# Optimization experiments

Measured on AMD Instinct MI355X. Metric: run time of the kernel, lower is better.

Reference implementation:

```python
import jax, jax.numpy as jnp
import numpy as np

B, N1, R12, R23 = 1, 4096, 4, 4
N2, N3 = N1 * R12, N1 * R12 * R23
D, F, H, NCLS, K = 1024, 512, 256, 4, 256


def setup_inputs() -> dict:
    key = jax.random.key(0)
    ks = jax.random.split(key, 10)
    s = 0.02
    return {
        "x1": jax.random.normal(ks[0], (B, N1, D), jnp.float32),
        "x2": jax.random.normal(ks[1], (B, N2, D), jnp.float32),
        "x3": jax.random.normal(ks[2], (B, N3, D), jnp.float32),
        # 3 fc layers (low/mid/high mag): Linear(D->F)
        "fcW": (jax.random.normal(ks[3], (3, D, F), jnp.float32) * s),
        "fcb": jnp.zeros((3, F), jnp.float32),
        # 5 gated-attention modules: 0=ga_low,1=ga_mid,2=ga_high,3=aux_low,4=aux_mid
        "gaWa": (jax.random.normal(ks[4], (5, F, H), jnp.float32) * s),
        "gaba": jnp.zeros((5, H), jnp.float32),
        "gaWb": (jax.random.normal(ks[5], (5, F, H), jnp.float32) * s),
        "gabb": jnp.zeros((5, H), jnp.float32),
        "gaWc": (jax.random.normal(ks[6], (5, H, 1), jnp.float32) * s),
        "gabc": jnp.zeros((5, 1), jnp.float32),
        "Wh": (jax.random.normal(ks[7], (F, NCLS), jnp.float32) * s),
        "bh": jnp.zeros((NCLS,), jnp.float32),
        "k_sample": K,
    }


def _ga(x, i, Wa, ba, Wb, bb, Wc, bc):
    # GatedAttention: tanh branch * sigmoid branch -> Linear(H->1); returns (B,N)
    a = jnp.tanh(x @ Wa[i] + ba[i])
    g = jax.nn.sigmoid(x @ Wb[i] + bb[i])
    return ((a * g) @ Wc[i] + bc[i])[..., 0]


def _block_gather(x, idx, ratio):
    # Equivalent to einsum('bkn,bnd->bkd', kron(one_hot(idx), eye(ratio)), x):
    # pick contiguous blocks of `ratio` rows for each selected coarse index.
    b, n, d = x.shape
    xb = x.reshape(b, n // ratio, ratio, d)
    out = jnp.take_along_axis(xb, idx[:, :, None, None], axis=1)  # (B,k,ratio,D)
    return out.reshape(b, idx.shape[1] * ratio, d)


def reference(x1, x2, x3, fcW, fcb, gaWa, gaba, gaWb, gabb, gaWc, gabc, Wh, bh, k_sample):
    ga = (gaWa, gaba, gaWb, gabb, gaWc, gabc)
    n1, n2, n3 = x1.shape[1], x2.shape[1], x3.shape[1]

    # --- low mag ---
    h1 = jax.nn.relu(x1 @ fcW[0] + fcb[0])                    # (B,N1,F)
    A1 = jax.nn.softmax(_ga(h1, 0, *ga), axis=-1)             # (B,N1)
    M1 = jnp.einsum('bn,bnf->bf', A1, h1)                     # (B,F)
    A1_aux = jax.nn.softmax(_ga(h1, 3, *ga), axis=-1)
    k1 = min(n1, int(k_sample))
    idx1 = jnp.sort(jax.lax.top_k(A1_aux, k1)[1], axis=-1)    # (B,k1)

    # zoom: gather selected blocks from mid and high mag features
    x2s = _block_gather(x2, idx1, n2 // n1)                   # (B,k1*R12,D)
    x3s = _block_gather(x3, idx1, n3 // n1)                   # (B,k1*R12*R23,D)

    # --- mid mag ---
    h2 = jax.nn.relu(x2s @ fcW[1] + fcb[1])
    A2 = jax.nn.softmax(_ga(h2, 1, *ga), axis=-1)
    M2 = jnp.einsum('bn,bnf->bf', A2, h2)
    A2_aux = jax.nn.softmax(_ga(h2, 4, *ga), axis=-1)
    k2 = min(h2.shape[1], int(k_sample))
    idx2 = jnp.sort(jax.lax.top_k(A2_aux, k2)[1], axis=-1)

    x3s2 = _block_gather(x3s, idx2, n3 // n2)                 # (B,k2*R23,D)

    # --- high mag ---
    h3 = jax.nn.relu(x3s2 @ fcW[2] + fcb[2])
    A3 = jax.nn.softmax(_ga(h3, 2, *ga), axis=-1)
    M3 = jnp.einsum('bn,bnf->bf', A3, h3)

    M = M1 + M2 + M3                                           # (B,F)
    logits = M @ Wh + bh                                       # (B,NCLS)
    return logits
```

## Files before the change

### kernel.cpp

```cpp
#include <hip/hip_runtime.h>
#include <hip/hip_bf16.h>
#include <math.h>


typedef __attribute__((ext_vector_type(8))) short short8;
typedef __attribute__((ext_vector_type(4))) float float4a;

__device__ __forceinline__ ushort f2bf(float f) {
    unsigned u = __float_as_uint(f);
    return (ushort)((u + 0x7fffu + ((u >> 16) & 1u)) >> 16);
}
__device__ __forceinline__ uint pk2(float a, float b) {
    __hip_bfloat162 t = __float22bfloat162_rn(make_float2(a, b));
    uint u; __builtin_memcpy(&u, &t, 4); return u;
}
__device__ __forceinline__ float aload(const float* p) {
    return __hip_atomic_load(p, __ATOMIC_RELAXED, __HIP_MEMORY_SCOPE_AGENT);
}

template<int SPLIT>
__global__ __launch_bounds__(256) void zm_hgemm(
    const float* __restrict__ A, int lda,
    const int* __restrict__ rowmap,
    const ushort* __restrict__ Bt,
    const float* __restrict__ bias,
    float* __restrict__ Cf, ushort* __restrict__ Cb, int ldc, int K)
{
    __shared__ ushort As[128 * 40];
    __shared__ ushort Bs[64 * 40];
    const int tid = threadIdx.x;
    const int brow = blockIdx.y << 7;
    const int bcol = blockIdx.x << 6;
    const int kbeg = SPLIT ? ((int)blockIdx.z << 8) : 0;
    const int kend = SPLIT ? kbeg + 256 : K;

    const int sr = tid >> 1;
    const int sk = (tid & 1) << 4;
    int arow = brow + sr;
    if (rowmap) arow = rowmap[arow];
    const float* Ap = A + (size_t)arow * lda;

    const int bn = tid >> 2;
    const int bk = (tid & 3) << 3;
    const ushort* Bp = Bt + (size_t)(bcol + bn) * K + bk;

    const int w = tid >> 6;
    const int wm = (w >> 1) << 6;
    const int wn = (w & 1) << 5;
    const int lane = tid & 63;
    const int lm = lane & 15;
    const int lq = lane >> 4;

    float4a acc[4][2] = {};

    for (int k0 = kbeg; k0 < kend; k0 += 32) {
        const float* ap = Ap + k0 + sk;
        float4 v0 = *(const float4*)(ap);
        float4 v1 = *(const float4*)(ap + 4);
        float4 v2 = *(const float4*)(ap + 8);
        float4 v3 = *(const float4*)(ap + 12);
        uint4 p0, p1;
        p0.x = pk2(v0.x, v0.y); p0.y = pk2(v0.z, v0.w);
        p0.z = pk2(v1.x, v1.y); p0.w = pk2(v1.z, v1.w);
        p1.x = pk2(v2.x, v2.y); p1.y = pk2(v2.z, v2.w);
        p1.z = pk2(v3.x, v3.y); p1.w = pk2(v3.z, v3.w);
        *(uint4*)&As[sr * 40 + sk]     = p0;
        *(uint4*)&As[sr * 40 + sk + 8] = p1;
        *(uint4*)&Bs[bn * 40 + bk] = *(const uint4*)(Bp + k0);
        __syncthreads();
        short8 afr[4], bfr[2];
#pragma unroll
        for (int mt = 0; mt < 4; mt++)
            afr[mt] = *(const short8*)&As[(wm + mt * 16 + lm) * 40 + lq * 8];
#pragma unroll
        for (int nt = 0; nt < 2; nt++)
            bfr[nt] = *(const short8*)&Bs[(wn + nt * 16 + lm) * 40 + lq * 8];
#pragma unroll
        for (int mt = 0; mt < 4; mt++)
#pragma unroll
            for (int nt = 0; nt < 2; nt++)
                acc[mt][nt] = __builtin_amdgcn_mfma_f32_16x16x32_bf16(
                    afr[mt], bfr[nt], acc[mt][nt], 0, 0, 0);
        __syncthreads();
    }

#pragma unroll
    for (int mt = 0; mt < 4; mt++) {
#pragma unroll
        for (int nt = 0; nt < 2; nt++) {
            int gc = bcol + wn + nt * 16 + lm;
            float bv = bias[gc];
            if (SPLIT && blockIdx.z != 0) bv = 0.0f;
#pragma unroll
            for (int r = 0; r < 4; r++) {
                int gr = brow + wm + mt * 16 + lq * 4 + r;
                float v = acc[mt][nt][r] + bv;
                if (SPLIT) {
                    atomicAdd(&Cf[(size_t)gr * ldc + gc], v);
                } else {
                    v = fmaxf(v, 0.0f);
                    Cf[(size_t)gr * ldc + gc] = v;
                    Cb[(size_t)gr * ldc + gc] = f2bf(v);
                }
            }
        }
    }
}

template<int AMODE>
__global__ __launch_bounds__(256) void zm_sgemm(
    const void* __restrict__ Av, int lda,
    const ushort* __restrict__ Bt,
    const float* __restrict__ bint,
    const float* __restrict__ wc0, const float* __restrict__ wc1,
    float* __restrict__ sMain, float* __restrict__ sAux,
    float* __restrict__ statsOut, int* __restrict__ cnt2, int lastBlk)
{
    __shared__ ushort As[64 * 40];
    __shared__ ushort Bs[64 * 40];
    __shared__ float part[4][64];
    const int tid = threadIdx.x;
    const int brow = blockIdx.y << 6;
    const int bcol = blockIdx.x << 6;

    const int sr = tid >> 2;
    const int sk = (tid & 3) << 3;
    const float*  Af = (const float*)Av;
    const ushort* Ab = (const ushort*)Av;
    const ushort* Bp = Bt + (size_t)(bcol + sr) * 512 + sk;

    const int w = tid >> 6;
    const int wn = w << 4;
    const int lane = tid & 63;
    const int lm = lane & 15;
    const int lq = lane >> 4;

    float4a acc[4] = {};

    for (int k0 = 0; k0 < 512; k0 += 32) {
        if (AMODE == 0) {
            *(uint4*)&As[sr * 40 + sk] =
                *(const uint4*)(Ab + (size_t)(brow + sr) * lda + k0 + sk);
        } else {
            const float* ap = Af + (size_t)(brow + sr) * lda + k0 + sk;
            float4 v0 = *(const float4*)ap;
            float4 v1 = *(const float4*)(ap + 4);
            v0.x = fmaxf(v0.x, 0.f); v0.y = fmaxf(v0.y, 0.f);
            v0.z = fmaxf(v0.z, 0.f); v0.w = fmaxf(v0.w, 0.f);
            v1.x = fmaxf(v1.x, 0.f); v1.y = fmaxf(v1.y, 0.f);
            v1.z = fmaxf(v1.z, 0.f); v1.w = fmaxf(v1.w, 0.f);
            uint4 pk;
            pk.x = pk2(v0.x, v0.y); pk.y = pk2(v0.z, v0.w);
            pk.z = pk2(v1.x, v1.y); pk.w = pk2(v1.z, v1.w);
            *(uint4*)&As[sr * 40 + sk] = pk;
        }
        *(uint4*)&Bs[sr * 40 + sk] = *(const uint4*)(Bp + k0);
        __syncthreads();
        short8 bfr = *(const short8*)&Bs[(wn + lm) * 40 + lq * 8];
#pragma unroll
        for (int mt = 0; mt < 4; mt++) {
            short8 afr = *(const short8*)&As[(mt * 16 + lm) * 40 + lq * 8];
            acc[mt] = __builtin_amdgcn_mfma_f32_16x16x32_bf16(afr, bfr, acc[mt], 0, 0, 0);
        }
        __syncthreads();
    }

    const int gc = bcol + wn + lm;
    const float* wcp = (gc >= 512) ? wc1 : wc0;
    const float wcv = wcp[(gc & 511) >> 1];
    const float bv = bint[gc];
    const bool odd = (gc & 1);
    float* sp = (bcol >= 512) ? sAux : sMain;

#pragma unroll
    for (int mt = 0; mt < 4; mt++) {
        float red[4];
#pragma unroll
        for (int r = 0; r < 4; r++) {
            float v = acc[mt][r] + bv;
            float x = odd ? (1.0f / (1.0f + expf(-v))) : tanhf(v);
            float prt = __shfl_xor(x, 1);
            float ctr = odd ? 0.0f : (x * prt * wcv);
            ctr += __shfl_xor(ctr, 1);
            ctr += __shfl_xor(ctr, 2);
            ctr += __shfl_xor(ctr, 4);
            ctr += __shfl_xor(ctr, 8);
            red[r] = ctr;
        }
        if (lm == 0) {
#pragma unroll
            for (int r = 0; r < 4; r++) part[w][mt * 16 + lq * 4 + r] = red[r];
        }
    }
    __syncthreads();
    if (tid < 64) {
        float tot = part[0][tid] + part[1][tid] + part[2][tid] + part[3][tid];
        atomicAdd(&sp[brow + tid], tot);
    }

    if (statsOut) {
        __threadfence();
        __shared__ int lastf;
        if (tid == 0)
            lastf = (__hip_atomic_fetch_add(cnt2, 1, __ATOMIC_ACQ_REL,
                                            __HIP_MEMORY_SCOPE_AGENT) == lastBlk);
        __syncthreads();
        if (lastf) {
            float* red = (float*)part;
            float vv[4];
            float mx = -3.4e38f;
#pragma unroll
            for (int j = 0; j < 4; j++) {
                vv[j] = aload(&sMain[tid + j * 256]);
                mx = fmaxf(mx, vv[j]);
            }
            red[tid] = mx; __syncthreads();
            for (int o = 128; o > 0; o >>= 1) {
                if (tid < o) red[tid] = fmaxf(red[tid], red[tid + o]);
                __syncthreads();
            }
            mx = red[0]; __syncthreads();
            float z = 0.0f;
#pragma unroll
            for (int j = 0; j < 4; j++) z += expf(vv[j] - mx);
            red[tid] = z; __syncthreads();
            for (int o = 128; o > 0; o >>= 1) {
                if (tid < o) red[tid] += red[tid + o];
                __syncthreads();
            }
            if (tid == 0) { statsOut[0] = mx; statsOut[1] = red[0]; }
        }
    }
}

__global__ __launch_bounds__(1024) void zm_topk(
    const float* __restrict__ sa, const float* __restrict__ sm, int n,
    const int* __restrict__ idx_prev,
    int* __restrict__ idx_out, int* __restrict__ rm_out,
    float* __restrict__ stOut)
{
    __shared__ float redf[1024];
    __shared__ int hist[256];
    __shared__ int idxbuf[256];
    __shared__ int wsum[16];
    __shared__ int bcastB, bcastAbove;
    const int bs = 1024;
    const int tid = threadIdx.x;

    if (blockIdx.x == 1) {
        float mx = -3.4e38f;
        for (int i = tid; i < n; i += bs) mx = fmaxf(mx, sm[i]);
        redf[tid] = mx; __syncthreads();
        for (int o = 512; o > 0; o >>= 1) {
            if (tid < o) redf[tid] = fmaxf(redf[tid], redf[tid + o]);
            __syncthreads();
        }
        mx = redf[0]; __syncthreads();
        float z = 0.0f;
        for (int i = tid; i < n; i += bs) z += expf(sm[i] - mx);
        redf[tid] = z; __syncthreads();
        for (int o = 512; o > 0; o >>= 1) {
            if (tid < o) redf[tid] += redf[tid + o];
            __syncthreads();
        }
        if (tid == 0) { stOut[0] = mx; stOut[1] = redf[0]; }
        return;
    }

    const int ept = n >> 10;
    const int lane = tid & 63;
    unsigned key[4];
#pragma unroll
    for (int e = 0; e < 4; e++) key[e] = 0;
    for (int e = 0; e < ept; e++) {
        unsigned u = __float_as_uint(sa[tid * ept + e]);
        key[e] = (u & 0x80000000u) ? ~u : (u | 0x80000000u);
    }

    unsigned prefix = 0;
    int remaining = 256;
    for (int pass = 0; pass < 4; pass++) {
        const int shift = 24 - pass * 8;
        if (tid < 256) hist[tid] = 0;
        __syncthreads();
        for (int e = 0; e < ept; e++) {
            unsigned k = key[e];
            bool ok = (pass == 0) || ((k >> (shift + 8)) == (prefix >> (shift + 8)));
            if (ok) atomicAdd(&hist[(k >> shift) & 0xff], 1);
        }
        __syncthreads();
        if (tid < 64) {
            int h0 = hist[lane * 4 + 0], h1 = hist[lane * 4 + 1];
            int h2 = hist[lane * 4 + 2], h3 = hist[lane * 4 + 3];
            int q = h0 + h1 + h2 + h3;
            int suf = q;
#pragma unroll
            for (int o = 1; o < 64; o <<= 1) {
                int v = __shfl_down(suf, o);
                if (lane + o < 64) suf += v;
            }
            int above = suf - q;
            int c3 = above + h3;
            int c2 = c3 + h2;
            int c1 = c2 + h1;
            int c0 = c1 + h0;
            int cc[4]  = {c0, c1, c2, c3};
            int nxt[4] = {c1, c2, c3, above};
#pragma unroll
            for (int j = 0; j < 4; j++)
                if (cc[j] >= remaining && nxt[j] < remaining) {
                    bcastB = lane * 4 + j;
                    bcastAbove = nxt[j];
                }
        }
        __syncthreads();
        prefix |= ((unsigned)bcastB) << shift;
        remaining -= bcastAbove;
        __syncthreads();
    }
    const unsigned T = prefix;
    const int m = remaining;

    int gt = 0, eq = 0;
    for (int e = 0; e < ept; e++) { gt += (key[e] > T); eq += (key[e] == T); }
    int packed = (gt << 16) | eq;
    int incl = packed;
#pragma unroll
    for (int o = 1; o < 64; o <<= 1) {
        int v = __shfl_up(incl, o);
        if (lane >= o) incl += v;
    }
    if (lane == 63) wsum[tid >> 6] = incl;
    __syncthreads();
    if (tid < 64) {
        int v = (tid < 16) ? wsum[tid] : 0;
        int s = v;
#pragma unroll
        for (int o = 1; o < 16; o <<= 1) {
            int t2 = __shfl_up(s, o);
            if (tid >= o) s += t2;
        }
        if (tid < 16) wsum[tid] = s - v;
    }
    __syncthreads();
    int base = wsum[tid >> 6] + incl - packed;
    int gt_before = base >> 16;
    int eq_before = base & 0xffff;
    for (int e = 0; e < ept; e++) {
        if (key[e] > T) {
            int eqa = (eq_before < m) ? eq_before : m;
            idxbuf[gt_before + eqa] = tid * ept + e;
            gt_before++;
        } else if (key[e] == T) {
            if (eq_before < m) idxbuf[gt_before + eq_before] = tid * ept + e;
            eq_before++;
        }
    }
    __syncthreads();
    if (tid < 256) idx_out[tid] = idxbuf[tid];
    int t = idxbuf[tid >> 2] * 4 + (tid & 3);
    rm_out[tid] = idx_prev ? (idx_prev[t >> 4] * 16 + (t & 15)) : t;
}

__global__ __launch_bounds__(256) void zm_prep(
    const float* __restrict__ fcW,
    const float* __restrict__ gaWa, const float* __restrict__ gaWb,
    const float* __restrict__ gaba, const float* __restrict__ gabb,
    ushort* __restrict__ fc_t, ushort* __restrict__ gint,
    float* __restrict__ bint, float4* __restrict__ zbase, int zn4)
{
    const int b = blockIdx.x;
    const int tid = threadIdx.x;
    if (b >= 2817) {
        float4 z4 = make_float4(0.f, 0.f, 0.f, 0.f);
        for (int i = (b - 2817) * 256 + tid; i < zn4; i += 64 * 256)
            zbase[i] = z4;
        return;
    }
    if (b == 2816) {
        for (int i = tid; i < 2560; i += 256) {
            int n, head;
            if (i < 1024)      { n = i;        head = (n >> 9) ? 3 : 0; }
            else if (i < 2048) { n = i - 1024; head = (n >> 9) ? 4 : 1; }
            else               { n = i - 2048; head = 2; }
            int h = (n & 511) >> 1;
            const float* src = (n & 1) ? gabb : gaba;
            bint[i] = src[head * 256 + h];
        }
        return;
    }
    __shared__ ushort tile[32][33];
    const int c = tid & 31, r8 = tid >> 5;
    if (b < 1536) {
        int mat = b >> 9, rem = b & 511;
        int tk = rem >> 4, tn = rem & 15;
        const float* src = fcW + (size_t)mat * 1024 * 512;
        ushort* dst = fc_t + (size_t)mat * 512 * 1024;
        int k0 = tk * 32, n0 = tn * 32;
#pragma unroll
        for (int it = 0; it < 4; it++) {
            int r = r8 + it * 8;
            tile[r][c] = f2bf(src[(size_t)(k0 + r) * 512 + n0 + c]);
        }
        __syncthreads();
#pragma unroll
        for (int it = 0; it < 4; it++) {
            int r = r8 + it * 8;
            dst[(size_t)(n0 + r) * 1024 + k0 + c] = tile[c][r];
        }
    } else {
        int idx = b - 1536;
        int mat = idx >> 7, rem = idx & 127;
        int tk = rem >> 3, th = rem & 7;
        int head = mat >> 1, br = mat & 1;
        const float* src = (br ? gaWb : gaWa) + (size_t)head * 512 * 256;
        ushort* dstb; int off;
        if (head == 0)      { dstb = gint;              off = 0;   }
        else if (head == 1) { dstb = gint + 1024 * 512; off = 0;   }
        else if (head == 2) { dstb = gint + 2048 * 512; off = 0;   }
        else if (head == 3) { dstb = gint;              off = 512; }
        else                { dstb = gint + 1024 * 512; off = 512; }
        int k0 = tk * 32, h0 = th * 32;
#pragma unroll
        for (int it = 0; it < 4; it++) {
            int r = r8 + it * 8;
            tile[r][c] = f2bf(src[(size_t)(k0 + r) * 256 + h0 + c]);
        }
        __syncthreads();
#pragma unroll
        for (int it = 0; it < 4; it++) {
            int r = r8 + it * 8;
            dstb[(size_t)(off + 2 * (h0 + r) + br) * 512 + k0 + c] = tile[c][r];
        }
    }
}

__global__ __launch_bounds__(256) void zm_final(
    const float* __restrict__ h1f, const float* __restrict__ h2f,
    const float* __restrict__ h3f,
    const float* __restrict__ s1, const float* __restrict__ s2,
    const float* __restrict__ s3,
    const float* __restrict__ st, float* __restrict__ Mbuf,
    int* __restrict__ cnt,
    const float* __restrict__ Wh, const float* __restrict__ bh,
    float* __restrict__ out)
{
    const int tid = threadIdx.x;
    const int b = blockIdx.x;
    const float* h; const float* s; const float* stp; int r0, rl;
    if (b < 64)      { h = h1f; s = s1; stp = st;     r0 = b * 64;        rl = 0; }
    else if (b < 80) { h = h2f; s = s2; stp = st + 2; r0 = (b - 64) * 64; rl = 1; }
    else             { h = h3f; s = s3; stp = st + 4; r0 = (b - 80) * 64; rl = 1; }
    const float mx = stp[0];
    const float invZ = 1.0f / stp[1];
    float a0 = 0.0f, a1 = 0.0f;
    for (int r = 0; r < 64; r++) {
        int n = r0 + r;
        float wgt = expf(s[n] - mx) * invZ;
        float v0 = h[(size_t)n * 512 + tid];
        float v1 = h[(size_t)n * 512 + 256 + tid];
        if (rl) { v0 = fmaxf(v0, 0.f); v1 = fmaxf(v1, 0.f); }
        a0 += wgt * v0; a1 += wgt * v1;
    }
    atomicAdd(&Mbuf[tid], a0);
    atomicAdd(&Mbuf[tid + 256], a1);
    __threadfence();
    __shared__ int lastf;
    if (tid == 0)
        lastf = (__hip_atomic_fetch_add(cnt, 1, __ATOMIC_ACQ_REL,
                                        __HIP_MEMORY_SCOPE_AGENT) == 95);
    __syncthreads();
    if (lastf) {
        const int c = tid >> 6, lane = tid & 63;
        float pacc = 0.0f;
        for (int f = lane; f < 512; f += 64)
            pacc += aload(&Mbuf[f]) * Wh[f * 4 + c];
        for (int o = 32; o > 0; o >>= 1) pacc += __shfl_down(pacc, o);
        if (lane == 0) out[c] = pacc + bh[c];
    }
}

extern "C" void kernel_launch(void* const* d_in, const int* in_sizes, int n_in,
                              void* d_out, int out_size, void* d_ws, size_t ws_size,
                              hipStream_t stream)
{
    const float* x1   = (const float*)d_in[0];
    const float* x2   = (const float*)d_in[1];
    const float* x3   = (const float*)d_in[2];
    const float* fcW  = (const float*)d_in[3];
    const float* fcb  = (const float*)d_in[4];
    const float* gaWa = (const float*)d_in[5];
    const float* gaba = (const float*)d_in[6];
    const float* gaWb = (const float*)d_in[7];
    const float* gabb = (const float*)d_in[8];
    const float* gaWc = (const float*)d_in[9];
    const float* Wh   = (const float*)d_in[11];
    const float* bh   = (const float*)d_in[12];
    float* out = (float*)d_out;

    char* p = (char*)d_ws;
    float*  h1f  = (float*)p;
    ushort* h1b  = (ushort*)(p + 8388608);
    ushort* fc_t = (ushort*)(p + 12582912);
    ushort* gint = (ushort*)(p + 15728640);
    float*  bint = (float*)(p + 18350080);
    float*  st   = (float*)(p + 18360320);
    int*    idx1 = (int*)(p + 18360352);
    int*    idx2 = (int*)(p + 18361376);
    int*    rm2  = (int*)(p + 18362400);
    int*    rm3  = (int*)(p + 18366496);
    char*   zbase = p + 18370592;
    float*  h2f  = (float*)zbase;
    float*  h3f  = (float*)(zbase + 2097152);
    float*  s1   = (float*)(zbase + 4194304);
    float*  s1a  = (float*)(zbase + 4210688);
    float*  s2   = (float*)(zbase + 4227072);
    float*  s2a  = (float*)(zbase + 4231168);
    float*  s3   = (float*)(zbase + 4235264);
    float*  Mbuf = (float*)(zbase + 4239360);
    int*    cnt  = (int*)(zbase + 4241408);
    const int ZN4 = 4241424 / 16;

    zm_prep<<<2881, 256, 0, stream>>>(fcW, gaWa, gaWb, gaba, gabb,
                                      fc_t, gint, bint, (float4*)zbase, ZN4);
    zm_hgemm<0><<<dim3(8, 32), 256, 0, stream>>>(x1, 1024, nullptr, fc_t, fcb,
                                                 h1f, h1b, 512, 1024);
    zm_sgemm<0><<<dim3(16, 64), 256, 0, stream>>>(h1b, 512, gint, bint,
                                                  gaWc, gaWc + 3 * 256,
                                                  s1, s1a, nullptr, nullptr, 0);
    zm_topk<<<2, 1024, 0, stream>>>(s1a, s1, 4096, nullptr, idx1, rm2, st);
    zm_hgemm<1><<<dim3(8, 8, 4), 256, 0, stream>>>(x2, 1024, rm2,
                                                   fc_t + 512 * 1024, fcb + 512,
                                                   h2f, nullptr, 512, 1024);
    zm_sgemm<1><<<dim3(16, 16), 256, 0, stream>>>(h2f, 512, gint + 1024 * 512,
                                                  bint + 1024,
                                                  gaWc + 256, gaWc + 4 * 256,
                                                  s2, s2a, nullptr, nullptr, 0);
    zm_topk<<<2, 1024, 0, stream>>>(s2a, s2, 1024, idx1, idx2, rm3, st + 2);
    zm_hgemm<1><<<dim3(8, 8, 4), 256, 0, stream>>>(x3, 1024, rm3,
                                                   fc_t + 2 * 512 * 1024, fcb + 1024,
                                                   h3f, nullptr, 512, 1024);
    zm_sgemm<1><<<dim3(8, 16), 256, 0, stream>>>(h3f, 512, gint + 2048 * 512,
                                                 bint + 2048,
                                                 gaWc + 2 * 256, gaWc + 2 * 256,
                                                 s3, s3, st + 4, cnt + 1, 127);
    zm_final<<<96, 256, 0, stream>>>(h1f, h2f, h3f, s1, s2, s3, st, Mbuf, cnt,
                                     Wh, bh, out);
}
```

Before: 540.4 us.

## Double-buffer GEMM tiles, fuse top-k into score GEMM, vectorize prep, widen final

Both GEMM kernels now use double-buffered shared-memory tiles and prefetch the next K slice into registers, which removes one barrier per iteration. The separate top-k/softmax-stats kernel is folded into the tail of the score GEMM: the last-arriving block does the radix select and builds the row maps, saving two launches. The weight-transpose prep switches to float4 loads and ushort4 stores, and the final reduction uses twice as many blocks with half the rows each. The fused top-k now runs on a single 256-thread block instead of 1024 threads, so that serial tail may take longer; the new completion counters (cnt+2, cnt+3) must sit inside the zeroed region.

```diff
diff --git a/kernel.cpp b/kernel.cpp
--- a/kernel.cpp
+++ b/kernel.cpp
@@ -26,13 +26,14 @@
     const float* __restrict__ bias,
     float* __restrict__ Cf, ushort* __restrict__ Cb, int ldc, int K)
 {
-    __shared__ ushort As[128 * 40];
-    __shared__ ushort Bs[64 * 40];
+    __shared__ ushort As[2][128 * 40];
+    __shared__ ushort Bs[2][64 * 40];
     const int tid = threadIdx.x;
     const int brow = blockIdx.y << 7;
     const int bcol = blockIdx.x << 6;
     const int kbeg = SPLIT ? ((int)blockIdx.z << 8) : 0;
     const int kend = SPLIT ? kbeg + 256 : K;
+    const int nsteps = (kend - kbeg) >> 5;
 
     const int sr = tid >> 1;
     const int sk = (tid & 1) << 4;
@@ -53,35 +54,48 @@
 
     float4a acc[4][2] = {};
 
-    for (int k0 = kbeg; k0 < kend; k0 += 32) {
-        const float* ap = Ap + k0 + sk;
-        float4 v0 = *(const float4*)(ap);
-        float4 v1 = *(const float4*)(ap + 4);
-        float4 v2 = *(const float4*)(ap + 8);
-        float4 v3 = *(const float4*)(ap + 12);
+    float4 v0, v1, v2, v3; uint4 bld;
+    {
+        const float* ap = Ap + kbeg + sk;
+        v0 = *(const float4*)(ap);
+        v1 = *(const float4*)(ap + 4);
+        v2 = *(const float4*)(ap + 8);
+        v3 = *(const float4*)(ap + 12);
+        bld = *(const uint4*)(Bp + kbeg);
+    }
+
+    for (int s = 0; s < nsteps; s++) {
+        const int cur = s & 1;
         uint4 p0, p1;
         p0.x = pk2(v0.x, v0.y); p0.y = pk2(v0.z, v0.w);
         p0.z = pk2(v1.x, v1.y); p0.w = pk2(v1.z, v1.w);
         p1.x = pk2(v2.x, v2.y); p1.y = pk2(v2.z, v2.w);
         p1.z = pk2(v3.x, v3.y); p1.w = pk2(v3.z, v3.w);
-        *(uint4*)&As[sr * 40 + sk]     = p0;
-        *(uint4*)&As[sr * 40 + sk + 8] = p1;
-        *(uint4*)&Bs[bn * 40 + bk] = *(const uint4*)(Bp + k0);
-        __syncthreads();
+        *(uint4*)&As[cur][sr * 40 + sk]     = p0;
+        *(uint4*)&As[cur][sr * 40 + sk + 8] = p1;
+        *(uint4*)&Bs[cur][bn * 40 + bk] = bld;
+        __syncthreads();
+        if (s + 1 < nsteps) {
+            const float* ap = Ap + kbeg + ((s + 1) << 5) + sk;
+            v0 = *(const float4*)(ap);
+            v1 = *(const float4*)(ap + 4);
+            v2 = *(const float4*)(ap + 8);
+            v3 = *(const float4*)(ap + 12);
+            bld = *(const uint4*)(Bp + kbeg + ((s + 1) << 5));
+        }
         short8 afr[4], bfr[2];
 #pragma unroll
         for (int mt = 0; mt < 4; mt++)
-            afr[mt] = *(const short8*)&As[(wm + mt * 16 + lm) * 40 + lq * 8];
+            afr[mt] = *(const short8*)&As[cur][(wm + mt * 16 + lm) * 40 + lq * 8];
 #pragma unroll
         for (int nt = 0; nt < 2; nt++)
-            bfr[nt] = *(const short8*)&Bs[(wn + nt * 16 + lm) * 40 + lq * 8];
+            bfr[nt] = *(const short8*)&Bs[cur][(wn + nt * 16 + lm) * 40 + lq * 8];
 #pragma unroll
         for (int mt = 0; mt < 4; mt++)
 #pragma unroll
             for (int nt = 0; nt < 2; nt++)
                 acc[mt][nt] = __builtin_amdgcn_mfma_f32_16x16x32_bf16(
                     afr[mt], bfr[nt], acc[mt][nt], 0, 0, 0);
-        __syncthreads();
     }
 
 #pragma unroll
@@ -107,17 +121,19 @@
     }
 }
 
-template<int AMODE>
+template<int AMODE, int NS, int DOTOPK>
 __global__ __launch_bounds__(256) void zm_sgemm(
     const void* __restrict__ Av, int lda,
     const ushort* __restrict__ Bt,
     const float* __restrict__ bint,
     const float* __restrict__ wc0, const float* __restrict__ wc1,
     float* __restrict__ sMain, float* __restrict__ sAux,
+    const int* __restrict__ idx_prev,
+    int* __restrict__ idx_out, int* __restrict__ rm_out,
     float* __restrict__ statsOut, int* __restrict__ cnt2, int lastBlk)
 {
-    __shared__ ushort As[64 * 40];
-    __shared__ ushort Bs[64 * 40];
+    __shared__ ushort As[2][64 * 40];
+    __shared__ ushort Bs[2][64 * 40];
     __shared__ float part[4][64];
     const int tid = threadIdx.x;
     const int brow = blockIdx.y << 6;
@@ -137,14 +153,22 @@
 
     float4a acc[4] = {};
 
-    for (int k0 = 0; k0 < 512; k0 += 32) {
+    uint4 aldu; float4 af0, af1; uint4 bld;
+    if (AMODE == 0) {
+        aldu = *(const uint4*)(Ab + (size_t)(brow + sr) * lda + sk);
+    } else {
+        const float* ap = Af + (size_t)(brow + sr) * lda + sk;
+        af0 = *(const float4*)ap;
+        af1 = *(const float4*)(ap + 4);
+    }
+    bld = *(const uint4*)(Bp);
+
+    for (int s = 0; s < 16; s++) {
+        const int cur = s & 1;
         if (AMODE == 0) {
-            *(uint4*)&As[sr * 40 + sk] =
-                *(const uint4*)(Ab + (size_t)(brow + sr) * lda + k0 + sk);
+            *(uint4*)&As[cur][sr * 40 + sk] = aldu;
         } else {
-            const float* ap = Af + (size_t)(brow + sr) * lda + k0 + sk;
-            float4 v0 = *(const float4*)ap;
-            float4 v1 = *(const float4*)(ap + 4);
+            float4 v0 = af0, v1 = af1;
             v0.x = fmaxf(v0.x, 0.f); v0.y = fmaxf(v0.y, 0.f);
             v0.z = fmaxf(v0.z, 0.f); v0.w = fmaxf(v0.w, 0.f);
             v1.x = fmaxf(v1.x, 0.f); v1.y = fmaxf(v1.y, 0.f);
@@ -152,17 +176,27 @@
             uint4 pk;
             pk.x = pk2(v0.x, v0.y); pk.y = pk2(v0.z, v0.w);
             pk.z = pk2(v1.x, v1.y); pk.w = pk2(v1.z, v1.w);
-            *(uint4*)&As[sr * 40 + sk] = pk;
-        }
-        *(uint4*)&Bs[sr * 40 + sk] = *(const uint4*)(Bp + k0);
-        __syncthreads();
-        short8 bfr = *(const short8*)&Bs[(wn + lm) * 40 + lq * 8];
+            *(uint4*)&As[cur][sr * 40 + sk] = pk;
+        }
+        *(uint4*)&Bs[cur][sr * 40 + sk] = bld;
+        __syncthreads();
+        if (s + 1 < 16) {
+            const int k1 = (s + 1) << 5;
+            if (AMODE == 0) {
+                aldu = *(const uint4*)(Ab + (size_t)(brow + sr) * lda + k1 + sk);
+            } else {
+                const float* ap = Af + (size_t)(brow + sr) * lda + k1 + sk;
+                af0 = *(const float4*)ap;
+                af1 = *(const float4*)(ap + 4);
+            }
+            bld = *(const uint4*)(Bp + k1);
+        }
+        short8 bfr = *(const short8*)&Bs[cur][(wn + lm) * 40 + lq * 8];
 #pragma unroll
         for (int mt = 0; mt < 4; mt++) {
-            short8 afr = *(const short8*)&As[(mt * 16 + lm) * 40 + lq * 8];
+            short8 afr = *(const short8*)&As[cur][(mt * 16 + lm) * 40 + lq * 8];
             acc[mt] = __builtin_amdgcn_mfma_f32_16x16x32_bf16(afr, bfr, acc[mt], 0, 0, 0);
         }
-        __syncthreads();
     }
 
     const int gc = bcol + wn + lm;
@@ -198,168 +232,139 @@
         atomicAdd(&sp[brow + tid], tot);
     }
 
-    if (statsOut) {
-        __threadfence();
-        __shared__ int lastf;
-        if (tid == 0)
-            lastf = (__hip_atomic_fetch_add(cnt2, 1, __ATOMIC_ACQ_REL,
-                                            __HIP_MEMORY_SCOPE_AGENT) == lastBlk);
-        __syncthreads();
-        if (lastf) {
-            float* red = (float*)part;
-            float vv[4];
-            float mx = -3.4e38f;
-#pragma unroll
-            for (int j = 0; j < 4; j++) {
-                vv[j] = aload(&sMain[tid + j * 256]);
-                mx = fmaxf(mx, vv[j]);
-            }
-            red[tid] = mx; __syncthreads();
-            for (int o = 128; o > 0; o >>= 1) {
-                if (tid < o) red[tid] = fmaxf(red[tid], red[tid + o]);
-                __syncthreads();
-            }
-            mx = red[0]; __syncthreads();
-            float z = 0.0f;
-#pragma unroll
-            for (int j = 0; j < 4; j++) z += expf(vv[j] - mx);
-            red[tid] = z; __syncthreads();
-            for (int o = 128; o > 0; o >>= 1) {
-                if (tid < o) red[tid] += red[tid + o];
-                __syncthreads();
-            }
-            if (tid == 0) { statsOut[0] = mx; statsOut[1] = red[0]; }
-        }
-    }
-}
-
-__global__ __launch_bounds__(1024) void zm_topk(
-    const float* __restrict__ sa, const float* __restrict__ sm, int n,
-    const int* __restrict__ idx_prev,
-    int* __restrict__ idx_out, int* __restrict__ rm_out,
-    float* __restrict__ stOut)
-{
-    __shared__ float redf[1024];
-    __shared__ int hist[256];
-    __shared__ int idxbuf[256];
-    __shared__ int wsum[16];
-    __shared__ int bcastB, bcastAbove;
-    const int bs = 1024;
-    const int tid = threadIdx.x;
-
-    if (blockIdx.x == 1) {
+    __threadfence();
+    __shared__ int lastf;
+    if (tid == 0)
+        lastf = (__hip_atomic_fetch_add(cnt2, 1, __ATOMIC_ACQ_REL,
+                                        __HIP_MEMORY_SCOPE_AGENT) == lastBlk);
+    __syncthreads();
+    if (!lastf) return;
+
+    {
+        constexpr int SEPT = NS / 256;
+        float* redf = &part[0][0];
+        float vv[SEPT];
         float mx = -3.4e38f;
-        for (int i = tid; i < n; i += bs) mx = fmaxf(mx, sm[i]);
+#pragma unroll
+        for (int j = 0; j < SEPT; j++) {
+            vv[j] = aload(&sMain[tid + j * 256]);
+            mx = fmaxf(mx, vv[j]);
+        }
         redf[tid] = mx; __syncthreads();
-        for (int o = 512; o > 0; o >>= 1) {
+        for (int o = 128; o > 0; o >>= 1) {
             if (tid < o) redf[tid] = fmaxf(redf[tid], redf[tid + o]);
             __syncthreads();
         }
         mx = redf[0]; __syncthreads();
         float z = 0.0f;
-        for (int i = tid; i < n; i += bs) z += expf(sm[i] - mx);
+#pragma unroll
+        for (int j = 0; j < SEPT; j++) z += expf(vv[j] - mx);
         redf[tid] = z; __syncthreads();
-        for (int o = 512; o > 0; o >>= 1) {
+        for (int o = 128; o > 0; o >>= 1) {
             if (tid < o) redf[tid] += redf[tid + o];
             __syncthreads();
         }
-        if (tid == 0) { stOut[0] = mx; stOut[1] = redf[0]; }
-        return;
-    }
-
-    const int ept = n >> 10;
-    const int lane = tid & 63;
-    unsigned key[4];
-#pragma unroll
-    for (int e = 0; e < 4; e++) key[e] = 0;
-    for (int e = 0; e < ept; e++) {
-        unsigned u = __float_as_uint(sa[tid * ept + e]);
-        key[e] = (u & 0x80000000u) ? ~u : (u | 0x80000000u);
-    }
-
-    unsigned prefix = 0;
-    int remaining = 256;
-    for (int pass = 0; pass < 4; pass++) {
-        const int shift = 24 - pass * 8;
-        if (tid < 256) hist[tid] = 0;
-        __syncthreads();
-        for (int e = 0; e < ept; e++) {
-            unsigned k = key[e];
-            bool ok = (pass == 0) || ((k >> (shift + 8)) == (prefix >> (shift + 8)));
-            if (ok) atomicAdd(&hist[(k >> shift) & 0xff], 1);
-        }
-        __syncthreads();
-        if (tid < 64) {
-            int h0 = hist[lane * 4 + 0], h1 = hist[lane * 4 + 1];
-            int h2 = hist[lane * 4 + 2], h3 = hist[lane * 4 + 3];
-            int q = h0 + h1 + h2 + h3;
-            int suf = q;
-#pragma unroll
-            for (int o = 1; o < 64; o <<= 1) {
-                int v = __shfl_down(suf, o);
-                if (lane + o < 64) suf += v;
+        if (tid == 0) { statsOut[0] = mx; statsOut[1] = redf[0]; }
+    }
+
+    if constexpr (DOTOPK) {
+        constexpr int EPT = NS / 256;
+        __shared__ int hist[256];
+        __shared__ int idxbuf[256];
+        __shared__ int wsum[4];
+        __shared__ int bcastB, bcastAbove;
+        const int w4 = tid >> 6;
+
+        unsigned key[EPT];
+#pragma unroll
+        for (int e = 0; e < EPT; e++) {
+            unsigned u = __float_as_uint(aload(&sAux[tid * EPT + e]));
+            key[e] = (u & 0x80000000u) ? ~u : (u | 0x80000000u);
+        }
+        __syncthreads();
+
+        unsigned prefix = 0;
+        int remaining = 256;
+        for (int pass = 0; pass < 4; pass++) {
+            const int shift = 24 - pass * 8;
+            hist[tid] = 0;
+            __syncthreads();
+#pragma unroll
+            for (int e = 0; e < EPT; e++) {
+                unsigned k = key[e];
+                bool ok = (pass == 0) ||
+                          ((k >> (shift + 8)) == (prefix >> (shift + 8)));
+                if (ok) atomicAdd(&hist[(k >> shift) & 0xff], 1);
             }
-            int above = suf - q;
-            int c3 = above + h3;
-            int c2 = c3 + h2;
-            int c1 = c2 + h1;
-            int c0 = c1 + h0;
-            int cc[4]  = {c0, c1, c2, c3};
-            int nxt[4] = {c1, c2, c3, above};
-#pragma unroll
-            for (int j = 0; j < 4; j++)
-                if (cc[j] >= remaining && nxt[j] < remaining) {
-                    bcastB = lane * 4 + j;
-                    bcastAbove = nxt[j];
+            __syncthreads();
+            if (tid < 64) {
+                int h0 = hist[tid * 4 + 0], h1 = hist[tid * 4 + 1];
+                int h2 = hist[tid * 4 + 2], h3 = hist[tid * 4 + 3];
+                int q = h0 + h1 + h2 + h3;
+                int suf = q;
+#pragma unroll
+                for (int o = 1; o < 64; o <<= 1) {
+                    int v = __shfl_down(suf, o);
+                    if (tid + o < 64) suf += v;
                 }
-        }
-        __syncthreads();
-        prefix |= ((unsigned)bcastB) << shift;
-        remaining -= bcastAbove;
-        __syncthreads();
-    }
-    const unsigned T = prefix;
-    const int m = remaining;
-
-    int gt = 0, eq = 0;
-    for (int e = 0; e < ept; e++) { gt += (key[e] > T); eq += (key[e] == T); }
-    int packed = (gt << 16) | eq;
-    int incl = packed;
-#pragma unroll
-    for (int o = 1; o < 64; o <<= 1) {
-        int v = __shfl_up(incl, o);
-        if (lane >= o) incl += v;
-    }
-    if (lane == 63) wsum[tid >> 6] = incl;
-    __syncthreads();
-    if (tid < 64) {
-        int v = (tid < 16) ? wsum[tid] : 0;
-        int s = v;
-#pragma unroll
-        for (int o = 1; o < 16; o <<= 1) {
-            int t2 = __shfl_up(s, o);
-            if (tid >= o) s += t2;
-        }
-        if (tid < 16) wsum[tid] = s - v;
-    }
-    __syncthreads();
-    int base = wsum[tid >> 6] + incl - packed;
-    int gt_before = base >> 16;
-    int eq_before = base & 0xffff;
-    for (int e = 0; e < ept; e++) {
-        if (key[e] > T) {
-            int eqa = (eq_before < m) ? eq_before : m;
-            idxbuf[gt_before + eqa] = tid * ept + e;
-            gt_before++;
-        } else if (key[e] == T) {
-            if (eq_before < m) idxbuf[gt_before + eq_before] = tid * ept + e;
-            eq_before++;
-        }
-    }
-    __syncthreads();
-    if (tid < 256) idx_out[tid] = idxbuf[tid];
-    int t = idxbuf[tid >> 2] * 4 + (tid & 3);
-    rm_out[tid] = idx_prev ? (idx_prev[t >> 4] * 16 + (t & 15)) : t;
+                int above = suf - q;
+                int c3 = above + h3;
+                int c2 = c3 + h2;
+                int c1 = c2 + h1;
+                int c0 = c1 + h0;
+                int cc[4]  = {c0, c1, c2, c3};
+                int nxt[4] = {c1, c2, c3, above};
+#pragma unroll
+                for (int j = 0; j < 4; j++)
+                    if (cc[j] >= remaining && nxt[j] < remaining) {
+                        bcastB = tid * 4 + j;
+                        bcastAbove = nxt[j];
+                    }
+            }
+            __syncthreads();
+            prefix |= ((unsigned)bcastB) << shift;
+            remaining -= bcastAbove;
+            __syncthreads();
+        }
+        const unsigned T = prefix;
+        const int m = remaining;
+
+        int gt = 0, eq = 0;
+#pragma unroll
+        for (int e = 0; e < EPT; e++) { gt += (key[e] > T); eq += (key[e] == T); }
+        int packed = (gt << 16) | eq;
+        int incl = packed;
+#pragma unroll
+        for (int o = 1; o < 64; o <<= 1) {
+            int v = __shfl_up(incl, o);
+            if (lane >= o) incl += v;
+        }
+        if (lane == 63) wsum[w4] = incl;
+        __syncthreads();
+        int wb = 0;
+#pragma unroll
+        for (int j = 0; j < 4; j++) if (j < w4) wb += wsum[j];
+        int base = wb + incl - packed;
+        int gt_before = base >> 16;
+        int eq_before = base & 0xffff;
+#pragma unroll
+        for (int e = 0; e < EPT; e++) {
+            if (key[e] > T) {
+                int eqa = (eq_before < m) ? eq_before : m;
+                idxbuf[gt_before + eqa] = tid * EPT + e;
+                gt_before++;
+            } else if (key[e] == T) {
+                if (eq_before < m) idxbuf[gt_before + eq_before] = tid * EPT + e;
+                eq_before++;
+            }
+        }
+        __syncthreads();
+        idx_out[tid] = idxbuf[tid];
+        for (int j = tid; j < 1024; j += 256) {
+            int t = idxbuf[j >> 2] * 4 + (j & 3);
+            rm_out[j] = idx_prev ? (idx_prev[t >> 4] * 16 + (t & 15)) : t;
+        }
+    }
 }
 
 __global__ __launch_bounds__(256) void zm_prep(
@@ -390,24 +395,24 @@
         return;
     }
     __shared__ ushort tile[32][33];
-    const int c = tid & 31, r8 = tid >> 5;
+    const int r = tid >> 3;
+    const int c4 = (tid & 7) << 2;
     if (b < 1536) {
         int mat = b >> 9, rem = b & 511;
         int tk = rem >> 4, tn = rem & 15;
         const float* src = fcW + (size_t)mat * 1024 * 512;
         ushort* dst = fc_t + (size_t)mat * 512 * 1024;
         int k0 = tk * 32, n0 = tn * 32;
-#pragma unroll
-        for (int it = 0; it < 4; it++) {
-            int r = r8 + it * 8;
-            tile[r][c] = f2bf(src[(size_t)(k0 + r) * 512 + n0 + c]);
-        }
-        __syncthreads();
-#pragma unroll
-        for (int it = 0; it < 4; it++) {
-            int r = r8 + it * 8;
-            dst[(size_t)(n0 + r) * 1024 + k0 + c] = tile[c][r];
-        }
+        float4 v = *(const float4*)&src[(size_t)(k0 + r) * 512 + n0 + c4];
+        tile[r][c4 + 0] = f2bf(v.x);
+        tile[r][c4 + 1] = f2bf(v.y);
+        tile[r][c4 + 2] = f2bf(v.z);
+        tile[r][c4 + 3] = f2bf(v.w);
+        __syncthreads();
+        ushort4 o;
+        o.x = tile[c4 + 0][r]; o.y = tile[c4 + 1][r];
+        o.z = tile[c4 + 2][r]; o.w = tile[c4 + 3][r];
+        *(ushort4*)&dst[(size_t)(n0 + r) * 1024 + k0 + c4] = o;
     } else {
         int idx = b - 1536;
         int mat = idx >> 7, rem = idx & 127;
@@ -421,17 +426,16 @@
         else if (head == 3) { dstb = gint;              off = 512; }
         else                { dstb = gint + 1024 * 512; off = 512; }
         int k0 = tk * 32, h0 = th * 32;
-#pragma unroll
-        for (int it = 0; it < 4; it++) {
-            int r = r8 + it * 8;
-            tile[r][c] = f2bf(src[(size_t)(k0 + r) * 256 + h0 + c]);
-        }
-        __syncthreads();
-#pragma unroll
-        for (int it = 0; it < 4; it++) {
-            int r = r8 + it * 8;
-            dstb[(size_t)(off + 2 * (h0 + r) + br) * 512 + k0 + c] = tile[c][r];
-        }
+        float4 v = *(const float4*)&src[(size_t)(k0 + r) * 256 + h0 + c4];
+        tile[r][c4 + 0] = f2bf(v.x);
+        tile[r][c4 + 1] = f2bf(v.y);
+        tile[r][c4 + 2] = f2bf(v.z);
+        tile[r][c4 + 3] = f2bf(v.w);
+        __syncthreads();
+        ushort4 o;
+        o.x = tile[c4 + 0][r]; o.y = tile[c4 + 1][r];
+        o.z = tile[c4 + 2][r]; o.w = tile[c4 + 3][r];
+        *(ushort4*)&dstb[(size_t)(off + 2 * (h0 + r) + br) * 512 + k0 + c4] = o;
     }
 }
 
@@ -448,13 +452,13 @@
     const int tid = threadIdx.x;
     const int b = blockIdx.x;
     const float* h; const float* s; const float* stp; int r0, rl;
-    if (b < 64)      { h = h1f; s = s1; stp = st;     r0 = b * 64;        rl = 0; }
-    else if (b < 80) { h = h2f; s = s2; stp = st + 2; r0 = (b - 64) * 64; rl = 1; }
-    else             { h = h3f; s = s3; stp = st + 4; r0 = (b - 80) * 64; rl = 1; }
+    if (b < 128)      { h = h1f; s = s1; stp = st;     r0 = b * 32;         rl = 0; }
+    else if (b < 160) { h = h2f; s = s2; stp = st + 2; r0 = (b - 128) * 32; rl = 1; }
+    else              { h = h3f; s = s3; stp = st + 4; r0 = (b - 160) * 32; rl = 1; }
     const float mx = stp[0];
     const float invZ = 1.0f / stp[1];
     float a0 = 0.0f, a1 = 0.0f;
-    for (int r = 0; r < 64; r++) {
+    for (int r = 0; r < 32; r++) {
         int n = r0 + r;
         float wgt = expf(s[n] - mx) * invZ;
         float v0 = h[(size_t)n * 512 + tid];
@@ -468,7 +472,7 @@
     __shared__ int lastf;
     if (tid == 0)
         lastf = (__hip_atomic_fetch_add(cnt, 1, __ATOMIC_ACQ_REL,
-                                        __HIP_MEMORY_SCOPE_AGENT) == 95);
+                                        __HIP_MEMORY_SCOPE_AGENT) == 191);
     __syncthreads();
     if (lastf) {
         const int c = tid >> 6, lane = tid & 63;
@@ -525,25 +529,21 @@
                                       fc_t, gint, bint, (float4*)zbase, ZN4);
     zm_hgemm<0><<<dim3(8, 32), 256, 0, stream>>>(x1, 1024, nullptr, fc_t, fcb,
                                                  h1f, h1b, 512, 1024);
-    zm_sgemm<0><<<dim3(16, 64), 256, 0, stream>>>(h1b, 512, gint, bint,
-                                                  gaWc, gaWc + 3 * 256,
-                                                  s1, s1a, nullptr, nullptr, 0);
-    zm_topk<<<2, 1024, 0, stream>>>(s1a, s1, 4096, nullptr, idx1, rm2, st);
+    zm_sgemm<0, 4096, 1><<<dim3(16, 64), 256, 0, stream>>>(
+        h1b, 512, gint, bint, gaWc, gaWc + 3 * 256,
+        s1, s1a, nullptr, idx1, rm2, st, cnt + 2, 1023);
     zm_hgemm<1><<<dim3(8, 8, 4), 256, 0, stream>>>(x2, 1024, rm2,
                                                    fc_t + 512 * 1024, fcb + 512,
                                                    h2f, nullptr, 512, 1024);
-    zm_sgemm<1><<<dim3(16, 16), 256, 0, stream>>>(h2f, 512, gint + 1024 * 512,
-                                                  bint + 1024,
-                                                  gaWc + 256, gaWc + 4 * 256,
-                                                  s2, s2a, nullptr, nullptr, 0);
-    zm_topk<<<2, 1024, 0, stream>>>(s2a, s2, 1024, idx1, idx2, rm3, st + 2);
+    zm_sgemm<1, 1024, 1><<<dim3(16, 16), 256, 0, stream>>>(
+        h2f, 512, gint + 1024 * 512, bint + 1024, gaWc + 256, gaWc + 4 * 256,
+        s2, s2a, idx1, idx2, rm3, st + 2, cnt + 3, 255);
     zm_hgemm<1><<<dim3(8, 8, 4), 256, 0, stream>>>(x3, 1024, rm3,
                                                    fc_t + 2 * 512 * 1024, fcb + 1024,
                                                    h3f, nullptr, 512, 1024);
-    zm_sgemm<1><<<dim3(8, 16), 256, 0, stream>>>(h3f, 512, gint + 2048 * 512,
-                                                 bint + 2048,
-                                                 gaWc + 2 * 256, gaWc + 2 * 256,
-                                                 s3, s3, st + 4, cnt + 1, 127);
-    zm_final<<<96, 256, 0, stream>>>(h1f, h2f, h3f, s1, s2, s3, st, Mbuf, cnt,
-                                     Wh, bh, out);
-}
+    zm_sgemm<1, 1024, 0><<<dim3(8, 16), 256, 0, stream>>>(
+        h3f, 512, gint + 2048 * 512, bint + 2048, gaWc + 2 * 256, gaWc + 2 * 256,
+        s3, s3, nullptr, nullptr, nullptr, st + 4, cnt + 1, 127);
+    zm_final<<<192, 256, 0, stream>>>(h1f, h2f, h3f, s1, s2, s3, st, Mbuf, cnt,
+                                      Wh, bh, out);
+}
```

Result: slower. 621.4 us (+15.0%).
